# Optimization experiments

Hardware: AMD Instinct MI355X
Metric: run time of the kernel (lower is better)

## Reference

```python
import math
import jax, jax.numpy as jnp
import numpy as np

N_STEPS = 4

def rotate_half(x):
    h = x.shape[-1] // 2
    return jnp.concatenate([-x[..., h:], x[..., :h]], axis=-1)

def setup_inputs() -> dict:
    key = jax.random.key(0)
    k0, k1, k2, k3 = jax.random.split(key, 4)
    B, N, F, D = 2, 4096, 512, 64
    features = jax.random.normal(k0, (B, N, F), jnp.float32)
    # standard RoPE tables, shape [N, D]
    inv_freq = 1.0 / (10000.0 ** (jnp.arange(0, D, 2, dtype=jnp.float32) / D))
    ang = jnp.arange(N, dtype=jnp.float32)[:, None] * inv_freq[None, :]  # [N, D/2]
    ang = jnp.concatenate([ang, ang], axis=-1)  # [N, D]
    cos, sin = jnp.cos(ang), jnp.sin(ang)
    # causal mask broadcast to [B, N, N]
    mask = jnp.broadcast_to(jnp.tril(jnp.ones((N, N), bool)), (B, N, N))
    s = 1.0 / math.sqrt(F)
    Wq = jax.random.normal(k1, (F, D), jnp.float32) * s
    Wk = jax.random.normal(k2, (F, D), jnp.float32) * s
    charge_w = jax.random.normal(k3, (F, 1), jnp.float32) * s
    charge_b = jnp.zeros((1,), jnp.float32)
    step_size = jnp.full((1,), 0.5, jnp.float32)
    charge_decay = jnp.full((1,), 0.3, jnp.float32)
    return dict(features=features, cos=cos, sin=sin, mask=mask, Wq=Wq, Wk=Wk,
                charge_w=charge_w, charge_b=charge_b,
                step_size=step_size, charge_decay=charge_decay)

def reference(features, cos, sin, mask, Wq, Wk, charge_w, charge_b, step_size, charge_decay):
    d_k = Wq.shape[-1]
    Q = jnp.einsum('bnf,fd->bnd', features, Wq)
    K = jnp.einsum('bnf,fd->bnd', features, Wk)
    c, s = cos[None, :, :], sin[None, :, :]  # broadcast over batch
    Q = Q * c + rotate_half(Q) * s
    K = K * c + rotate_half(K) * s
    compat = jnp.einsum('bnd,bmd->bnm', Q, K) / math.sqrt(d_k)  # [B,N,N]
    charge = jax.nn.sigmoid(jnp.einsum('bnf,fo->bno', features, charge_w)[..., 0] + charge_b[0])  # [B,N]
    neg_inf = jnp.asarray(-jnp.inf, compat.dtype)
    logits = jnp.where(mask, compat, neg_inf)
    ss = step_size[0]
    cd = charge_decay[0]
    for _ in range(N_STEPS):
        attn = jax.nn.softmax(logits, axis=-1)
        received = attn.sum(axis=-2)  # column sums, [B,N]
        charge = charge * (1.0 - cd * jax.nn.sigmoid(received - 1.0))
        energy = -compat * charge[..., :, None] * charge[..., None, :]
        logits = jnp.where(mask, logits - ss * energy, neg_inf)
    return jax.nn.softmax(logits, axis=-1)
```

## Files before the change

### kernel.cpp

```cpp
#include <hip/hip_runtime.h>
#include <math.h>

#define NTOK   4096
#define NFEAT  512
#define NDIM   64

__global__ __launch_bounds__(256) void qk_kernel(
    const float* __restrict__ feat, const float* __restrict__ cosb,
    const float* __restrict__ sinb, const float* __restrict__ Wq,
    const float* __restrict__ Wk, const float* __restrict__ cw,
    const float* __restrict__ cbp, float* __restrict__ Q, float* __restrict__ K,
    float* __restrict__ cur)
{
  __shared__ __align__(16) float smem[8 * NFEAT];
  const int tid  = threadIdx.x;
  const int row0 = blockIdx.x * 8;

  const float4* fb4 = (const float4*)(feat + (size_t)row0 * NFEAT);
  float4* sm4 = (float4*)smem;
#pragma unroll
  for (int i = tid; i < 8 * NFEAT / 4; i += 256) sm4[i] = fb4[i];
  __syncthreads();

  const int r   = tid >> 5;
  const int c   = tid & 31;
  const int isQ = (c < 16);
  const int d0  = (c & 15) * 4;
  const float* __restrict__ Wp = isQ ? Wq : Wk;
  const float* fr = smem + (r << 9);

  float a0 = 0.f, a1 = 0.f, a2 = 0.f, a3 = 0.f;
  for (int k = 0; k < NFEAT; ++k) {
    float fv = fr[k];
    float4 w = *(const float4*)(Wp + k * NDIM + d0);
    a0 = fmaf(fv, w.x, a0); a1 = fmaf(fv, w.y, a1);
    a2 = fmaf(fv, w.z, a2); a3 = fmaf(fv, w.w, a3);
  }

  float accc = 0.f;
#pragma unroll
  for (int j = 0; j < 16; ++j) accc = fmaf(fr[c + (j << 5)], cw[c + (j << 5)], accc);
#pragma unroll
  for (int o = 16; o > 0; o >>= 1) accc += __shfl_down(accc, o, 64);
  if (c == 0) {
    float cb = cbp[0];
    cur[row0 + r] = 1.f / (1.f + __expf(-(accc + cb)));
  }
  __syncthreads();

  float* sraw = smem;
  {
    float* dst = sraw + r * 132 + (isQ ? 0 : 64) + d0;
    dst[0] = a0; dst[1] = a1; dst[2] = a2; dst[3] = a3;
  }
  __syncthreads();

#pragma unroll
  for (int i = tid; i < 8 * NDIM; i += 256) {
    int rr = i >> 6, d = i & 63;
    int g = row0 + rr, n = g & (NTOK - 1);
    float cv = cosb[(n << 6) + d], sv = sinb[(n << 6) + d];
    float qv = sraw[rr * 132 + d];
    float qr = (d < 32) ? -sraw[rr * 132 + d + 32] : sraw[rr * 132 + d - 32];
    Q[(size_t)g * NDIM + d] = qv * cv + qr * sv;
    float kv = sraw[rr * 132 + 64 + d];
    float kr = (d < 32) ? -sraw[rr * 132 + 64 + d + 32] : sraw[rr * 132 + 64 + d - 32];
    K[(size_t)g * NDIM + d] = kv * cv + kr * sv;
  }
}

__global__ __launch_bounds__(256) void compat_kernel(
    const float* __restrict__ Q, const float* __restrict__ K, float* __restrict__ C)
{
  __shared__ __align__(16) float Qs[32][132];
  __shared__ __align__(16) float Ks[32][132];
  int p = blockIdx.x, b = 0;
  if (p >= 528) { b = 1; p -= 528; }
  int ti = (int)((sqrtf(8.f * p + 1.f) - 1.f) * 0.5f);
  while ((ti + 1) * (ti + 2) / 2 <= p) ++ti;
  while (ti * (ti + 1) / 2 > p) --ti;
  int tj = p - ti * (ti + 1) / 2;

  const int tid = threadIdx.x;
  const int ty = tid >> 4, tx = tid & 15;
  const int i0 = ty * 8, j0 = tx * 8;
  const size_t qbase = ((size_t)b * NTOK + (size_t)ti * 128) * NDIM;
  const size_t kbase = ((size_t)b * NTOK + (size_t)tj * 128) * NDIM;

  float acc[8][8];
#pragma unroll
  for (int ii = 0; ii < 8; ++ii)
#pragma unroll
    for (int jj = 0; jj < 8; ++jj) acc[ii][jj] = 0.f;

  for (int dk = 0; dk < NDIM; dk += 32) {
    __syncthreads();
    for (int i = tid; i < 128 * 32; i += 256) {
      int row = i >> 5, d = i & 31;
      Qs[d][row] = Q[qbase + (size_t)row * NDIM + dk + d];
      Ks[d][row] = K[kbase + (size_t)row * NDIM + dk + d];
    }
    __syncthreads();
#pragma unroll
    for (int d = 0; d < 32; ++d) {
      float4 q0 = *(const float4*)&Qs[d][i0];
      float4 q1 = *(const float4*)&Qs[d][i0 + 4];
      float4 k0 = *(const float4*)&Ks[d][j0];
      float4 k1 = *(const float4*)&Ks[d][j0 + 4];
      float av[8] = {q0.x, q0.y, q0.z, q0.w, q1.x, q1.y, q1.z, q1.w};
      float bv[8] = {k0.x, k0.y, k0.z, k0.w, k1.x, k1.y, k1.z, k1.w};
#pragma unroll
      for (int ii = 0; ii < 8; ++ii)
#pragma unroll
        for (int jj = 0; jj < 8; ++jj)
          acc[ii][jj] = fmaf(av[ii], bv[jj], acc[ii][jj]);
    }
  }
#pragma unroll
  for (int ii = 0; ii < 8; ++ii) {
    size_t grow = (size_t)b * NTOK + (size_t)ti * 128 + i0 + ii;
    float4 w0 = make_float4(acc[ii][0] * 0.125f, acc[ii][1] * 0.125f,
                            acc[ii][2] * 0.125f, acc[ii][3] * 0.125f);
    float4 w1 = make_float4(acc[ii][4] * 0.125f, acc[ii][5] * 0.125f,
                            acc[ii][6] * 0.125f, acc[ii][7] * 0.125f);
    *(float4*)&C[grow * NTOK + (size_t)tj * 128 + j0]     = w0;
    *(float4*)&C[grow * NTOK + (size_t)tj * 128 + j0 + 4] = w1;
  }
}

template <int T, bool FINAL>
__global__ __launch_bounds__(256) void sweep_kernel(
    float* __restrict__ CC, const float* __restrict__ cstep,
    const float* __restrict__ ssp, float* __restrict__ partial)
{
  __shared__ float cs[NTOK];
  const int tid  = threadIdx.x;
  const int lane = tid & 63;
  const int w    = tid >> 6;
  const int bid  = blockIdx.x;
  const int b    = bid >> 9;
  const int p    = bid & 511;
  const float ss = ssp[0];

  if (!FINAL) {
    for (int i = tid; i < NTOK; i += 256) cs[i] = 0.f;
    __syncthreads();
  }

  float* base = CC + ((size_t)b << 24);
  const float* planes = cstep + (b << 12);

  const int rows[2] = { (p << 2) + w, ((1023 - p) << 2) + w };

#pragma unroll
  for (int ri = 0; ri < 2; ++ri) {
    const int n = rows[ri];
    const int kmax = n >> 8;
    float* rowp = base + ((size_t)n << 12);

    float hs[T ? T : 1];
#pragma unroll
    for (int t = 0; t < T; ++t) hs[t] = ss * planes[t * 2 * NTOK + n];

    float4 e[16];
    float lsum = 0.f;
#pragma unroll
    for (int k = 0; k < 16; ++k) {
      if (k > kmax) continue;
      const int c = (k << 8) + (lane << 2);
      float4 cv = *(const float4*)(rowp + c);
      float f0 = 1.f, f1 = 1.f, f2 = 1.f, f3 = 1.f;
#pragma unroll
      for (int t = 0; t < T; ++t) {
        float4 ct = *(const float4*)(planes + t * 2 * NTOK + c);
        f0 = fmaf(ct.x, hs[t], f0); f1 = fmaf(ct.y, hs[t], f1);
        f2 = fmaf(ct.z, hs[t], f2); f3 = fmaf(ct.w, hs[t], f3);
      }
      float x0 = __expf(cv.x * f0);
      float x1 = __expf(cv.y * f1);
      float x2 = __expf(cv.z * f2);
      float x3 = __expf(cv.w * f3);
      e[k].x = (c     <= n) ? x0 : 0.f;
      e[k].y = (c + 1 <= n) ? x1 : 0.f;
      e[k].z = (c + 2 <= n) ? x2 : 0.f;
      e[k].w = (c + 3 <= n) ? x3 : 0.f;
      lsum += (e[k].x + e[k].y) + (e[k].z + e[k].w);
    }
#pragma unroll
    for (int o = 1; o < 64; o <<= 1) lsum += __shfl_xor(lsum, o, 64);
    const float inv = 1.f / lsum;

    if (FINAL) {
#pragma unroll
      for (int k = 0; k < 16; ++k) {
        const int c = (k << 8) + (lane << 2);
        float4 wv = make_float4(0.f, 0.f, 0.f, 0.f);
        if (k <= kmax)
          wv = make_float4(e[k].x * inv, e[k].y * inv, e[k].z * inv, e[k].w * inv);
        *(float4*)(rowp + c) = wv;
      }
    } else {
#pragma unroll
      for (int k = 0; k < 16; ++k) {
        if (k > kmax) continue;
        const int c = (k << 8) + (lane << 2);
        atomicAdd(&cs[c],     e[k].x * inv);
        atomicAdd(&cs[c + 1], e[k].y * inv);
        atomicAdd(&cs[c + 2], e[k].z * inv);
        atomicAdd(&cs[c + 3], e[k].w * inv);
      }
    }
  }

  if (!FINAL) {
    __syncthreads();
    const int len4 = (NTOK - 4 * p) >> 2;
    float4* pp = (float4*)(partial + ((size_t)bid << 12));
    const float4* cs4 = (const float4*)cs;
    for (int i = tid; i < len4; i += 256) pp[i] = cs4[i];
  }
}

__global__ __launch_bounds__(256) void fold_kernel(
    const float* __restrict__ partial, const float* __restrict__ cdp,
    float* __restrict__ cur, float* __restrict__ cstep, int step)
{
  __shared__ float s[4][64];
  const int tid = threadIdx.x;
  const int ml = tid & 63, seg = tid >> 6;
  const int idx = blockIdx.x * 64 + ml;
  const int b = idx >> 12, m = idx & (NTOK - 1);
  const int count = min(512, ((NTOK - 1 - m) >> 2) + 1);
  const float* pp = partial + (((size_t)b << 9) << 12) + m;
  float r = 0.f;
  for (int q = seg; q < count; q += 4) r += pp[(size_t)q << 12];
  s[seg][ml] = r;
  __syncthreads();
  if (seg == 0) {
    float rr = s[0][ml] + s[1][ml] + s[2][ml] + s[3][ml];
    float sig = 1.f / (1.f + __expf(-(rr - 1.f)));
    float c = cur[idx] * (1.f - cdp[0] * sig);
    cur[idx] = c;
    cstep[step * 2 * NTOK + idx] = c;
  }
}

extern "C" void kernel_launch(void* const* d_in, const int* in_sizes, int n_in,
                              void* d_out, int out_size, void* d_ws, size_t ws_size,
                              hipStream_t stream) {
  const float* feat = (const float*)d_in[0];
  const float* cosb = (const float*)d_in[1];
  const float* sinb = (const float*)d_in[2];
  const float* Wq  = (const float*)d_in[4];
  const float* Wk  = (const float*)d_in[5];
  const float* cw  = (const float*)d_in[6];
  const float* cbp = (const float*)d_in[7];
  const float* ssp = (const float*)d_in[8];
  const float* cdp = (const float*)d_in[9];
  float* out = (float*)d_out;

  float* ws      = (float*)d_ws;
  float* Q       = ws;
  float* K       = ws + 524288;
  float* cur     = ws + 1048576;
  float* cstep   = ws + 1056768;
  float* partial = ws + 1089536;

  qk_kernel<<<1024, 256, 0, stream>>>(feat, cosb, sinb, Wq, Wk, cw, cbp, Q, K, cur);
  compat_kernel<<<1056, 256, 0, stream>>>(Q, K, out);

  sweep_kernel<0, false><<<1024, 256, 0, stream>>>(out, cstep, ssp, partial);
  fold_kernel<<<128, 256, 0, stream>>>(partial, cdp, cur, cstep, 0);
  sweep_kernel<1, false><<<1024, 256, 0, stream>>>(out, cstep, ssp, partial);
  fold_kernel<<<128, 256, 0, stream>>>(partial, cdp, cur, cstep, 1);
  sweep_kernel<2, false><<<1024, 256, 0, stream>>>(out, cstep, ssp, partial);
  fold_kernel<<<128, 256, 0, stream>>>(partial, cdp, cur, cstep, 2);
  sweep_kernel<3, false><<<1024, 256, 0, stream>>>(out, cstep, ssp, partial);
  fold_kernel<<<128, 256, 0, stream>>>(partial, cdp, cur, cstep, 3);
  sweep_kernel<4, true><<<1024, 256, 0, stream>>>(out, cstep, ssp, nullptr);
}
```

Measured before the change: 842.7 us.

## Store compat matrix and charge planes in fp16 to halve sweep traffic

The compat kernel now writes the scaled QK scores as half precision into the second half of each output row. The four softmax sweeps read 8 halves per lane instead of 4 floats, and charge planes are also kept in fp16. Sweeps are memory-bound over the N×N matrix, so halving the bytes read per pass should cut bandwidth cost. The column-sum layout changes to a strided lane mapping, which the fold kernel un-permutes, and partials are now written in full. This risks precision loss in logits and exponentials (fp16 rounding of exp values), and it drops the causal-length trimming of partial writes.

```diff
diff --git a/kernel.cpp b/kernel.cpp
--- a/kernel.cpp
+++ b/kernel.cpp
@@ -1,9 +1,11 @@
 #include <hip/hip_runtime.h>
+#include <hip/hip_fp16.h>
 #include <math.h>
 
 #define NTOK   4096
 #define NFEAT  512
 #define NDIM   64
+
 
 __global__ __launch_bounds__(256) void qk_kernel(
     const float* __restrict__ feat, const float* __restrict__ cosb,
@@ -119,19 +121,21 @@
 #pragma unroll
   for (int ii = 0; ii < 8; ++ii) {
     size_t grow = (size_t)b * NTOK + (size_t)ti * 128 + i0 + ii;
-    float4 w0 = make_float4(acc[ii][0] * 0.125f, acc[ii][1] * 0.125f,
-                            acc[ii][2] * 0.125f, acc[ii][3] * 0.125f);
-    float4 w1 = make_float4(acc[ii][4] * 0.125f, acc[ii][5] * 0.125f,
-                            acc[ii][6] * 0.125f, acc[ii][7] * 0.125f);
-    *(float4*)&C[grow * NTOK + (size_t)tj * 128 + j0]     = w0;
-    *(float4*)&C[grow * NTOK + (size_t)tj * 128 + j0 + 4] = w1;
+    __half* chrow = (__half*)((char*)C + grow * 16384 + 8192);
+    __align__(16) __half2 hh[4];
+    hh[0] = __floats2half2_rn(acc[ii][0] * 0.125f, acc[ii][1] * 0.125f);
+    hh[1] = __floats2half2_rn(acc[ii][2] * 0.125f, acc[ii][3] * 0.125f);
+    hh[2] = __floats2half2_rn(acc[ii][4] * 0.125f, acc[ii][5] * 0.125f);
+    hh[3] = __floats2half2_rn(acc[ii][6] * 0.125f, acc[ii][7] * 0.125f);
+    *(float4*)(chrow + tj * 128 + j0) = *(const float4*)hh;
   }
 }
 
 template <int T, bool FINAL>
 __global__ __launch_bounds__(256) void sweep_kernel(
     float* __restrict__ CC, const float* __restrict__ cstep,
-    const float* __restrict__ ssp, float* __restrict__ partial)
+    const __half* __restrict__ csteph, const float* __restrict__ ssp,
+    float* __restrict__ partial)
 {
   __shared__ float cs[NTOK];
   const int tid  = threadIdx.x;
@@ -147,101 +151,131 @@
     __syncthreads();
   }
 
-  float* base = CC + ((size_t)b << 24);
-  const float* planes = cstep + (b << 12);
-
   const int rows[2] = { (p << 2) + w, ((1023 - p) << 2) + w };
 
 #pragma unroll
   for (int ri = 0; ri < 2; ++ri) {
     const int n = rows[ri];
-    const int kmax = n >> 8;
-    float* rowp = base + ((size_t)n << 12);
+    const int kmax = n >> 9;
+    const size_t slot = (size_t)((b << 12) + n);
+    const __half* rowh = (const __half*)((const char*)CC + (slot << 14) + 8192);
 
     float hs[T ? T : 1];
 #pragma unroll
-    for (int t = 0; t < T; ++t) hs[t] = ss * planes[t * 2 * NTOK + n];
-
-    float4 e[16];
+    for (int t = 0; t < T; ++t) hs[t] = ss * cstep[t * 2 * NTOK + (b << 12) + n];
+
+    __align__(16) __half2 e2[8][4];
     float lsum = 0.f;
 #pragma unroll
-    for (int k = 0; k < 16; ++k) {
+    for (int k = 0; k < 8; ++k) {
       if (k > kmax) continue;
-      const int c = (k << 8) + (lane << 2);
-      float4 cv = *(const float4*)(rowp + c);
-      float f0 = 1.f, f1 = 1.f, f2 = 1.f, f3 = 1.f;
+      const int c0 = (k << 9) + (lane << 3);
+      float4 raw = *(const float4*)(rowh + c0);
+      const __half2* hv = (const __half2*)&raw;
+      float2 v0 = __half22float2(hv[0]), v1 = __half22float2(hv[1]);
+      float2 v2 = __half22float2(hv[2]), v3 = __half22float2(hv[3]);
+      float f[8] = {1.f, 1.f, 1.f, 1.f, 1.f, 1.f, 1.f, 1.f};
 #pragma unroll
       for (int t = 0; t < T; ++t) {
-        float4 ct = *(const float4*)(planes + t * 2 * NTOK + c);
-        f0 = fmaf(ct.x, hs[t], f0); f1 = fmaf(ct.y, hs[t], f1);
-        f2 = fmaf(ct.z, hs[t], f2); f3 = fmaf(ct.w, hs[t], f3);
+        float4 pr = *(const float4*)(csteph + t * 2 * NTOK + (b << 12) + c0);
+        const __half2* pv = (const __half2*)&pr;
+        float2 c0f = __half22float2(pv[0]), c1f = __half22float2(pv[1]);
+        float2 c2f = __half22float2(pv[2]), c3f = __half22float2(pv[3]);
+        f[0] = fmaf(c0f.x, hs[t], f[0]); f[1] = fmaf(c0f.y, hs[t], f[1]);
+        f[2] = fmaf(c1f.x, hs[t], f[2]); f[3] = fmaf(c1f.y, hs[t], f[3]);
+        f[4] = fmaf(c2f.x, hs[t], f[4]); f[5] = fmaf(c2f.y, hs[t], f[5]);
+        f[6] = fmaf(c3f.x, hs[t], f[6]); f[7] = fmaf(c3f.y, hs[t], f[7]);
       }
-      float x0 = __expf(cv.x * f0);
-      float x1 = __expf(cv.y * f1);
-      float x2 = __expf(cv.z * f2);
-      float x3 = __expf(cv.w * f3);
-      e[k].x = (c     <= n) ? x0 : 0.f;
-      e[k].y = (c + 1 <= n) ? x1 : 0.f;
-      e[k].z = (c + 2 <= n) ? x2 : 0.f;
-      e[k].w = (c + 3 <= n) ? x3 : 0.f;
-      lsum += (e[k].x + e[k].y) + (e[k].z + e[k].w);
+      float x0 = __expf(v0.x * f[0]);
+      float x1 = __expf(v0.y * f[1]);
+      float x2 = __expf(v1.x * f[2]);
+      float x3 = __expf(v1.y * f[3]);
+      float x4 = __expf(v2.x * f[4]);
+      float x5 = __expf(v2.y * f[5]);
+      float x6 = __expf(v3.x * f[6]);
+      float x7 = __expf(v3.y * f[7]);
+      x0 = (c0     <= n) ? x0 : 0.f;  x1 = (c0 + 1 <= n) ? x1 : 0.f;
+      x2 = (c0 + 2 <= n) ? x2 : 0.f;  x3 = (c0 + 3 <= n) ? x3 : 0.f;
+      x4 = (c0 + 4 <= n) ? x4 : 0.f;  x5 = (c0 + 5 <= n) ? x5 : 0.f;
+      x6 = (c0 + 6 <= n) ? x6 : 0.f;  x7 = (c0 + 7 <= n) ? x7 : 0.f;
+      lsum += ((x0 + x1) + (x2 + x3)) + ((x4 + x5) + (x6 + x7));
+      e2[k][0] = __floats2half2_rn(x0, x1);
+      e2[k][1] = __floats2half2_rn(x2, x3);
+      e2[k][2] = __floats2half2_rn(x4, x5);
+      e2[k][3] = __floats2half2_rn(x6, x7);
     }
 #pragma unroll
     for (int o = 1; o < 64; o <<= 1) lsum += __shfl_xor(lsum, o, 64);
     const float inv = 1.f / lsum;
 
     if (FINAL) {
-#pragma unroll
-      for (int k = 0; k < 16; ++k) {
-        const int c = (k << 8) + (lane << 2);
-        float4 wv = make_float4(0.f, 0.f, 0.f, 0.f);
-        if (k <= kmax)
-          wv = make_float4(e[k].x * inv, e[k].y * inv, e[k].z * inv, e[k].w * inv);
-        *(float4*)(rowp + c) = wv;
+      float* orow = (float*)((char*)CC + (slot << 14));
+#pragma unroll
+      for (int k = 0; k < 8; ++k) {
+        const int c0 = (k << 9) + (lane << 3);
+        float4 wa = make_float4(0.f, 0.f, 0.f, 0.f);
+        float4 wb = make_float4(0.f, 0.f, 0.f, 0.f);
+        if (k <= kmax) {
+          float2 y0 = __half22float2(e2[k][0]), y1 = __half22float2(e2[k][1]);
+          float2 y2 = __half22float2(e2[k][2]), y3 = __half22float2(e2[k][3]);
+          wa = make_float4(y0.x * inv, y0.y * inv, y1.x * inv, y1.y * inv);
+          wb = make_float4(y2.x * inv, y2.y * inv, y3.x * inv, y3.y * inv);
+        }
+        *(float4*)(orow + c0)     = wa;
+        *(float4*)(orow + c0 + 4) = wb;
       }
     } else {
 #pragma unroll
-      for (int k = 0; k < 16; ++k) {
+      for (int k = 0; k < 8; ++k) {
         if (k > kmax) continue;
-        const int c = (k << 8) + (lane << 2);
-        atomicAdd(&cs[c],     e[k].x * inv);
-        atomicAdd(&cs[c + 1], e[k].y * inv);
-        atomicAdd(&cs[c + 2], e[k].z * inv);
-        atomicAdd(&cs[c + 3], e[k].w * inv);
+        float2 y0 = __half22float2(e2[k][0]), y1 = __half22float2(e2[k][1]);
+        float2 y2 = __half22float2(e2[k][2]), y3 = __half22float2(e2[k][3]);
+        float* csk = cs + (k << 9) + lane;
+        atomicAdd(csk,       y0.x * inv);
+        atomicAdd(csk + 64,  y0.y * inv);
+        atomicAdd(csk + 128, y1.x * inv);
+        atomicAdd(csk + 192, y1.y * inv);
+        atomicAdd(csk + 256, y2.x * inv);
+        atomicAdd(csk + 320, y2.y * inv);
+        atomicAdd(csk + 384, y3.x * inv);
+        atomicAdd(csk + 448, y3.y * inv);
       }
     }
   }
 
   if (!FINAL) {
     __syncthreads();
-    const int len4 = (NTOK - 4 * p) >> 2;
     float4* pp = (float4*)(partial + ((size_t)bid << 12));
     const float4* cs4 = (const float4*)cs;
-    for (int i = tid; i < len4; i += 256) pp[i] = cs4[i];
+    for (int i = tid; i < NTOK / 4; i += 256) pp[i] = cs4[i];
   }
 }
 
 __global__ __launch_bounds__(256) void fold_kernel(
     const float* __restrict__ partial, const float* __restrict__ cdp,
-    float* __restrict__ cur, float* __restrict__ cstep, int step)
+    float* __restrict__ cur, float* __restrict__ cstep,
+    __half* __restrict__ csteph, int step)
 {
-  __shared__ float s[4][64];
+  __shared__ float s[8][32];
   const int tid = threadIdx.x;
-  const int ml = tid & 63, seg = tid >> 6;
-  const int idx = blockIdx.x * 64 + ml;
+  const int ml = tid & 31, seg = tid >> 5;
+  const int idx = blockIdx.x * 32 + ml;
   const int b = idx >> 12, m = idx & (NTOK - 1);
-  const int count = min(512, ((NTOK - 1 - m) >> 2) + 1);
-  const float* pp = partial + (((size_t)b << 9) << 12) + m;
+  const int sm = ((m >> 9) << 9) | ((m & 7) << 6) | ((m >> 3) & 63);
+  const float* pb = partial + (((size_t)b << 9) << 12) + sm;
   float r = 0.f;
-  for (int q = seg; q < count; q += 4) r += pp[(size_t)q << 12];
+  for (int q = seg; q < 512; q += 8) r += pb[(size_t)q << 12];
   s[seg][ml] = r;
   __syncthreads();
   if (seg == 0) {
-    float rr = s[0][ml] + s[1][ml] + s[2][ml] + s[3][ml];
+    float rr = 0.f;
+#pragma unroll
+    for (int i = 0; i < 8; ++i) rr += s[i][ml];
     float sig = 1.f / (1.f + __expf(-(rr - 1.f)));
     float c = cur[idx] * (1.f - cdp[0] * sig);
     cur[idx] = c;
     cstep[step * 2 * NTOK + idx] = c;
+    csteph[step * 2 * NTOK + idx] = __float2half(c);
   }
 }
 
@@ -265,17 +299,18 @@
   float* cur     = ws + 1048576;
   float* cstep   = ws + 1056768;
   float* partial = ws + 1089536;
+  __half* csteph = (__half*)(ws + 5283840);
 
   qk_kernel<<<1024, 256, 0, stream>>>(feat, cosb, sinb, Wq, Wk, cw, cbp, Q, K, cur);
   compat_kernel<<<1056, 256, 0, stream>>>(Q, K, out);
 
-  sweep_kernel<0, false><<<1024, 256, 0, stream>>>(out, cstep, ssp, partial);
-  fold_kernel<<<128, 256, 0, stream>>>(partial, cdp, cur, cstep, 0);
-  sweep_kernel<1, false><<<1024, 256, 0, stream>>>(out, cstep, ssp, partial);
-  fold_kernel<<<128, 256, 0, stream>>>(partial, cdp, cur, cstep, 1);
-  sweep_kernel<2, false><<<1024, 256, 0, stream>>>(out, cstep, ssp, partial);
-  fold_kernel<<<128, 256, 0, stream>>>(partial, cdp, cur, cstep, 2);
-  sweep_kernel<3, false><<<1024, 256, 0, stream>>>(out, cstep, ssp, partial);
-  fold_kernel<<<128, 256, 0, stream>>>(partial, cdp, cur, cstep, 3);
-  sweep_kernel<4, true><<<1024, 256, 0, stream>>>(out, cstep, ssp, nullptr);
-}
+  sweep_kernel<0, false><<<1024, 256, 0, stream>>>(out, cstep, csteph, ssp, partial);
+  fold_kernel<<<256, 256, 0, stream>>>(partial, cdp, cur, cstep, csteph, 0);
+  sweep_kernel<1, false><<<1024, 256, 0, stream>>>(out, cstep, csteph, ssp, partial);
+  fold_kernel<<<256, 256, 0, stream>>>(partial, cdp, cur, cstep, csteph, 1);
+  sweep_kernel<2, false><<<1024, 256, 0, stream>>>(out, cstep, csteph, ssp, partial);
+  fold_kernel<<<256, 256, 0, stream>>>(partial, cdp, cur, cstep, csteph, 2);
+  sweep_kernel<3, false><<<1024, 256, 0, stream>>>(out, cstep, csteph, ssp, partial);
+  fold_kernel<<<256, 256, 0, stream>>>(partial, cdp, cur, cstep, csteph, 3);
+  sweep_kernel<4, true><<<1024, 256, 0, stream>>>(out, cstep, csteph, ssp, partial);
+}
```

Result: faster. 814.9 us (-3.3%).
